# Kernel optimization log

Measured on AMD Instinct MI355X. Metric: run time of the kernel, lower is better.

The kernel has to match this reference:

```python
import jax, jax.numpy as jnp
import numpy as np

D_MODEL, HEAD_DIM = 1024, 128

def setup_inputs() -> dict:
    key = jax.random.key(0)
    kx, kq, kk, kv = jax.random.split(key, 4)
    x = jax.random.normal(kx, (4, 4096, D_MODEL), dtype=jnp.float32)
    s = 1.0 / np.sqrt(D_MODEL)
    Wq = jax.random.normal(kq, (D_MODEL, HEAD_DIM), dtype=jnp.float32) * s
    Wk = jax.random.normal(kk, (D_MODEL, HEAD_DIM), dtype=jnp.float32) * s
    Wv = jax.random.normal(kv, (D_MODEL, HEAD_DIM), dtype=jnp.float32) * s
    return {"x": x, "Wq": Wq, "Wk": Wk, "Wv": Wv}

def reference(x, Wq, Wk, Wv):
    # x: [b, s, d_model]; Wq/Wk/Wv: [d_model, head_dim]
    q = jnp.einsum('bsd,dh->bsh', x, Wq)
    k = jnp.einsum('bsd,dh->bsh', x, Wk)
    v = jnp.einsum('bsd,dh->bsh', x, Wv)
    seq = x.shape[1]
    scale = 1.0 / jnp.sqrt(jnp.asarray(q.shape[-1], q.dtype))
    scores = jnp.einsum('bqh,bkh->bqk', q, k) * scale  # [b, s, s]
    causal = jnp.tril(jnp.ones((seq, seq), dtype=bool))
    scores = jnp.where(causal, scores, jnp.asarray(-jnp.inf, scores.dtype))
    attn = jax.nn.softmax(scores, axis=-1)
    return jnp.einsum('bqk,bkh->bqh', attn, v)
```

## Files before the change

### kernel.cpp

```cpp
#include <hip/hip_runtime.h>
#include <hip/hip_bf16.h>
#include <math.h>

#define D_MODEL 1024
#define HD 128
#define SEQ 4096

typedef __bf16 bf16x8 __attribute__((ext_vector_type(8)));
typedef float f32x4 __attribute__((ext_vector_type(4)));
typedef unsigned int u32;
typedef u32 u32x4 __attribute__((ext_vector_type(4)));

__device__ __forceinline__ unsigned short f2bf(float f) {
    union { float f; u32 u; } c; c.f = f;
    u32 u = c.u;
    u = (u + 0x7fffu + ((u >> 16) & 1u)) >> 16;
    return (unsigned short)u;
}
__device__ __forceinline__ u32 pk2(float a, float b) {
    __hip_bfloat162 h = __float22bfloat162_rn(make_float2(a, b));
    union { __hip_bfloat162 h; u32 u; } c; c.h = h; return c.u;
}
__device__ __forceinline__ void dma16(void* lds, const void* g) {
    __builtin_amdgcn_global_load_lds(
        (const __attribute__((address_space(1))) u32*)g,
        (__attribute__((address_space(3))) u32*)lds, 16, 0, 0);
}
__device__ __forceinline__ void drain_dma()  { __builtin_amdgcn_s_waitcnt(0x0F70); }

__global__ __launch_bounds__(256)
void wt_kernel(const float* __restrict__ Wq, const float* __restrict__ Wk,
               const float* __restrict__ Wv, unsigned short* __restrict__ Wt) {
    __shared__ float wsf[64][129];
    const int t = threadIdx.x;
    const int k0 = blockIdx.x * 64;
    const int mat = blockIdx.y;
    const float* W = (mat == 0) ? Wq : (mat == 1) ? Wk : Wv;
    const float sc = (mat == 0) ? (0.08838834764831845f * 1.4426950408889634f) : 1.0f;
    {
        const int r = t >> 2, c = (t & 3) * 32;
        const float* src = W + (size_t)(k0 + r) * HD + c;
        #pragma unroll
        for (int j = 0; j < 32; j += 4)
            *reinterpret_cast<f32x4*>(&wsf[r][c + j]) = *reinterpret_cast<const f32x4*>(src + j);
    }
    __syncthreads();
    const int n = t >> 1, ks = (t & 1) * 32;
    u32 ow[16];
    #pragma unroll
    for (int j = 0; j < 16; ++j)
        ow[j] = pk2(wsf[ks + 2 * j][n] * sc, wsf[ks + 2 * j + 1][n] * sc);
    unsigned short* dst = Wt + (size_t)(mat * HD + n) * D_MODEL + k0 + ks;
    #pragma unroll
    for (int j = 0; j < 4; ++j)
        *reinterpret_cast<u32x4*>(dst + j * 8) = (u32x4){ow[4*j], ow[4*j+1], ow[4*j+2], ow[4*j+3]};
}

__global__ __launch_bounds__(512, 2)
void proj_kernel(const float* __restrict__ x, const unsigned short* __restrict__ Wt,
                 unsigned short* __restrict__ Qb, unsigned short* __restrict__ Kb,
                 unsigned short* __restrict__ Vt) {
    __shared__ __align__(1024) char ps[131072];
    const int t = threadIdx.x;
    const int w = t >> 6, l = t & 63, li = l & 15, g2 = l >> 4;
    const int mh = w >> 2, nq = w & 3;
    const int rowbase = blockIdx.x * 64;

    const int lr = l >> 3, lg = l & 7;
    const int cg = lg ^ lr;
    const int wn_add = (cg >> 2) * 192;
    const int wkq = (cg & 3) * 8;

    auto stage = [&](int it) {
        const int k0 = it * 32;
        const int buf = it & 3;
        dma16(ps + buf * 8192 + w * 1024,
              x + (size_t)(rowbase + w * 8 + lr) * D_MODEL + k0 + cg * 4);
        #pragma unroll
        for (int j = 0; j < 3; ++j) {
            int r0 = w * 24 + j * 8;
            dma16(ps + 32768 + buf * 24576 + r0 * 128,
                  Wt + (size_t)(r0 + lr + wn_add) * D_MODEL + k0 + wkq);
        }
    };

    f32x4 acc[2][6];
    #pragma unroll
    for (int mt = 0; mt < 2; ++mt)
        #pragma unroll
        for (int nt = 0; nt < 6; ++nt) acc[mt][nt] = (f32x4){0.f, 0.f, 0.f, 0.f};

    stage(0); stage(1); stage(2);
    for (int it = 0; it < 32; ++it) {
        if (it < 30)       __builtin_amdgcn_s_waitcnt(0x0F78);
        else if (it == 30) __builtin_amdgcn_s_waitcnt(0x0F74);
        else               drain_dma();
        __syncthreads();
        if (it + 3 < 32) stage(it + 3);

        const char* xb = ps + (it & 3) * 8192;
        const char* wb = ps + 32768 + (it & 3) * 24576;

        bf16x8 bf[6];
        #pragma unroll
        for (int nt = 0; nt < 6; ++nt) {
            int r = (nq & 1) * 96 + nt * 16 + li;
            bf[nt] = *reinterpret_cast<const bf16x8*>(
                wb + r * 128 + ((((nq >> 1) * 4 + g2) ^ (li & 7)) * 16));
        }
        #pragma unroll
        for (int mt = 0; mt < 2; ++mt) {
            int row = mh * 32 + mt * 16 + li;
            int p0 = ((2 * g2) ^ (li & 7)) * 16;
            f32x4 x0 = *reinterpret_cast<const f32x4*>(xb + row * 128 + p0);
            f32x4 x1 = *reinterpret_cast<const f32x4*>(xb + row * 128 + (p0 ^ 16));
            union { u32 d[4]; bf16x8 v; } cva;
            cva.d[0] = pk2(x0[0], x0[1]); cva.d[1] = pk2(x0[2], x0[3]);
            cva.d[2] = pk2(x1[0], x1[1]); cva.d[3] = pk2(x1[2], x1[3]);
            bf16x8 af = cva.v;
            #pragma unroll
            for (int nt = 0; nt < 6; ++nt)
                acc[mt][nt] = __builtin_amdgcn_mfma_f32_16x16x32_bf16(af, bf[nt], acc[mt][nt], 0, 0, 0);
        }
    }

    #pragma unroll
    for (int nt = 0; nt < 6; ++nt) {
        const int c0 = nq * 96 + nt * 16;
        #pragma unroll
        for (int mt = 0; mt < 2; ++mt) {
            const int m0 = mh * 32 + mt * 16 + g2 * 4;
            if (c0 < 256) {
                unsigned short* P = (c0 < 128) ? Qb : Kb;
                const int col = (c0 < 128 ? c0 : c0 - 128) + li;
                #pragma unroll
                for (int r = 0; r < 4; ++r)
                    P[(size_t)(rowbase + m0 + r) * HD + col] = f2bf(acc[mt][nt][r]);
            } else {
                const int d = c0 - 256 + li;
                const int b_ = rowbase >> 12, s_ = (rowbase + m0) & 4095;
                ushort4 s4;
                s4.x = f2bf(acc[mt][nt][0]); s4.y = f2bf(acc[mt][nt][1]);
                s4.z = f2bf(acc[mt][nt][2]); s4.w = f2bf(acc[mt][nt][3]);
                *reinterpret_cast<ushort4*>(&Vt[((size_t)b_ * HD + d) * SEQ + s_]) = s4;
            }
        }
    }
}

__global__ __launch_bounds__(256, 2)
void attn_kernel(const unsigned short* __restrict__ Qb, const unsigned short* __restrict__ Kb,
                 const unsigned short* __restrict__ Vt, float* __restrict__ outO,
                 unsigned short* __restrict__ Obf, float* __restrict__ Lbuf) {
    __shared__ __align__(1024) char smem[73728];
    const int t = threadIdx.x;
    const int w = t >> 6, l = t & 63, li = l & 15, g2 = l >> 4;
    const int qh = w >> 1, kh = w & 1;
    const int b = blockIdx.x & 3;
    const int u = blockIdx.x >> 2;
    const int g = 63 - (u >> 2);
    const int c = u & 3;
    const int R = g + 1;
    const int ts = (c * R) >> 2, te = ((c + 1) * R) >> 2;
    const int q0 = g * 64;
    const size_t rowb = (size_t)b * SEQ;
    const int koff = kh * 32;

    const unsigned short* KbB = Kb + rowb * HD;
    const unsigned short* VtB = Vt + (size_t)b * HD * SEQ;
    const int vgran = ((l & 7) ^ (l >> 3)) * 8;

    auto stage = [&](int it, char* base) {
        const int j0 = it * 64;
        #pragma unroll
        for (int j = 0; j < 4; ++j) {
            int rK = w * 16 + 4 * j + (l >> 4);
            dma16(base + (w * 16 + 4 * j) * 256,
                  KbB + (size_t)(j0 + rK) * 128 + (((l & 15) ^ (rK & 7)) * 8));
            int rV = w * 32 + 8 * j + (l >> 3);
            dma16(base + 16384 + (w * 32 + 8 * j) * 128,
                  VtB + (size_t)rV * SEQ + j0 + vgran);
        }
    };

    bf16x8 qf[2][4];
    #pragma unroll
    for (int qt = 0; qt < 2; ++qt)
        #pragma unroll
        for (int ks = 0; ks < 4; ++ks)
            qf[qt][ks] = *reinterpret_cast<const bf16x8*>(
                Qb + (rowb + q0 + qh * 32 + qt * 16 + li) * HD + ks * 32 + g2 * 8);

    f32x4 acco[2][8];
    #pragma unroll
    for (int qt = 0; qt < 2; ++qt)
        #pragma unroll
        for (int dt = 0; dt < 8; ++dt) acco[qt][dt] = (f32x4){0.f, 0.f, 0.f, 0.f};
    float ls[2] = {0.f, 0.f};

    const int gV = ((4 * kh + g2) ^ (li & 7)) * 16;

    if (ts < te) stage(ts, smem);
    for (int it = ts; it < te; ++it) {
        char* cbuf = smem + ((it - ts) & 1) * 32768;
        char* nbuf = smem + (((it - ts) & 1) ^ 1) * 32768;
        drain_dma();
        __syncthreads();
        if (it + 1 < te) stage(it + 1, nbuf);

        f32x4 accs[2][2];
        #pragma unroll
        for (int qt = 0; qt < 2; ++qt)
            #pragma unroll
            for (int kt = 0; kt < 2; ++kt) accs[qt][kt] = (f32x4){0.f, 0.f, 0.f, 0.f};
        #pragma unroll
        for (int kt = 0; kt < 2; ++kt) {
            const char* kb = cbuf + (koff + kt * 16 + li) * 256;
            #pragma unroll
            for (int ks = 0; ks < 4; ++ks) {
                bf16x8 kf = *reinterpret_cast<const bf16x8*>(kb + (((4 * ks + g2) ^ (li & 7)) * 16));
                accs[0][kt] = __builtin_amdgcn_mfma_f32_16x16x32_bf16(kf, qf[0][ks], accs[0][kt], 0, 0, 0);
                accs[1][kt] = __builtin_amdgcn_mfma_f32_16x16x32_bf16(kf, qf[1][ks], accs[1][kt], 0, 0, 0);
            }
        }

        const bool masked = (it == g);
        #pragma unroll
        for (int qt = 0; qt < 2; ++qt) {
            const int prow = qh * 32 + qt * 16 + li;
            #pragma unroll
            for (int kt = 0; kt < 2; ++kt) {
                float p[4];
                #pragma unroll
                for (int r = 0; r < 4; ++r) {
                    float s = accs[qt][kt][r];
                    if (masked && (koff + kt * 16 + g2 * 4 + r > prow)) s = -INFINITY;
                    p[r] = __builtin_amdgcn_exp2f(s - 16.0f);
                    ls[qt] += p[r];
                }
                union { u32 d[2]; uint2 v; } pw;
                pw.d[0] = pk2(p[0], p[1]); pw.d[1] = pk2(p[2], p[3]);
                int gr = (kh * 4 + kt * 2 + (g2 >> 1)) ^ (prow & 7);
                *reinterpret_cast<uint2*>(
                    smem + 65536 + prow * 128 + gr * 16 + (g2 & 1) * 8) = pw.v;
            }
        }

        bf16x8 pb[2];
        #pragma unroll
        for (int qt = 0; qt < 2; ++qt) {
            const int prow = qh * 32 + qt * 16 + li;
            pb[qt] = *reinterpret_cast<const bf16x8*>(
                smem + 65536 + prow * 128 + (((kh * 4 + g2) ^ (prow & 7)) * 16));
        }
        #pragma unroll
        for (int dt = 0; dt < 8; ++dt) {
            bf16x8 va = *reinterpret_cast<const bf16x8*>(cbuf + 16384 + (dt * 16 + li) * 128 + gV);
            acco[0][dt] = __builtin_amdgcn_mfma_f32_16x16x32_bf16(va, pb[0], acco[0][dt], 0, 0, 0);
            acco[1][dt] = __builtin_amdgcn_mfma_f32_16x16x32_bf16(va, pb[1], acco[1][dt], 0, 0, 0);
        }
    }

    #pragma unroll
    for (int qt = 0; qt < 2; ++qt) {
        ls[qt] += __shfl_xor(ls[qt], 16);
        ls[qt] += __shfl_xor(ls[qt], 32);
    }

    float (*Osum)[132] = (float(*)[132])smem;
    float* Lsh = (float*)(smem + 33792);
    __syncthreads();
    if (l < 16) {
        Lsh[kh * 64 + qh * 32 + l]      = ls[0];
        Lsh[kh * 64 + qh * 32 + 16 + l] = ls[1];
    }
    if (kh == 0) {
        #pragma unroll
        for (int qt = 0; qt < 2; ++qt)
            #pragma unroll
            for (int dt = 0; dt < 8; ++dt)
                *reinterpret_cast<f32x4*>(
                    &Osum[qh * 32 + qt * 16 + li][dt * 16 + g2 * 4]) = acco[qt][dt];
    }
    __syncthreads();
    if (kh == 1) {
        #pragma unroll
        for (int qt = 0; qt < 2; ++qt)
            #pragma unroll
            for (int dt = 0; dt < 8; ++dt) {
                f32x4* p = reinterpret_cast<f32x4*>(
                    &Osum[qh * 32 + qt * 16 + li][dt * 16 + g2 * 4]);
                f32x4 v = *p;
                #pragma unroll
                for (int j = 0; j < 4; ++j) v[j] += acco[qt][dt][j];
                *p = v;
            }
    }
    __syncthreads();

    if (t < 64)
        Lbuf[(size_t)c * 16384 + rowb + q0 + t] = Lsh[t] + Lsh[64 + t];
    #pragma unroll
    for (int k = 0; k < 8; ++k) {
        int idx = t + k * 256;
        int row = idx >> 5, col = (idx & 31) * 4;
        f32x4 o = *reinterpret_cast<const f32x4*>(&Osum[row][col]);
        size_t grow = rowb + q0 + row;
        if (c == 3) {
            *reinterpret_cast<f32x4*>(&outO[grow * HD + col]) = o;
        } else {
            union { u32 d[2]; uint2 v; } pkd;
            pkd.d[0] = pk2(o[0], o[1]); pkd.d[1] = pk2(o[2], o[3]);
            *reinterpret_cast<uint2*>(&Obf[(size_t)c * 2097152 + grow * HD + col]) = pkd.v;
        }
    }
}

__global__ __launch_bounds__(256)
void merge_kernel(float* __restrict__ outO, const unsigned short* __restrict__ Obf,
                  const float* __restrict__ Lbuf) {
    int tid = blockIdx.x * 256 + threadIdx.x;
    #pragma unroll
    for (int k = 0; k < 4; ++k) {
        int idx = tid + k * 131072;
        int row = idx >> 5, col = (idx & 31) * 4;
        float lsum = Lbuf[row] + Lbuf[16384 + row] + Lbuf[32768 + row] + Lbuf[49152 + row];
        float inv = 1.f / lsum;
        f32x4 o = *reinterpret_cast<const f32x4*>(&outO[(size_t)row * HD + col]);
        #pragma unroll
        for (int cc = 0; cc < 3; ++cc) {
            ushort4 uu = *reinterpret_cast<const ushort4*>(
                &Obf[(size_t)cc * 2097152 + (size_t)row * HD + col]);
            union { u32 u; float f; } a, b2, c2, d2;
            a.u = (u32)uu.x << 16; b2.u = (u32)uu.y << 16;
            c2.u = (u32)uu.z << 16; d2.u = (u32)uu.w << 16;
            o[0] += a.f; o[1] += b2.f; o[2] += c2.f; o[3] += d2.f;
        }
        #pragma unroll
        for (int j = 0; j < 4; ++j) o[j] *= inv;
        *reinterpret_cast<f32x4*>(&outO[(size_t)row * HD + col]) = o;
    }
}

extern "C" void kernel_launch(void* const* d_in, const int* in_sizes, int n_in,
                              void* d_out, int out_size, void* d_ws, size_t ws_size,
                              hipStream_t stream) {
    const float* x  = (const float*)d_in[0];
    const float* Wq = (const float*)d_in[1];
    const float* Wk = (const float*)d_in[2];
    const float* Wv = (const float*)d_in[3];
    float* out = (float*)d_out;

    char* ws = (char*)d_ws;
    unsigned short* Qb  = (unsigned short*)(ws);
    unsigned short* Kb  = (unsigned short*)(ws + ((size_t)4  << 20));
    unsigned short* Vt  = (unsigned short*)(ws + ((size_t)8  << 20));
    unsigned short* Wt  = (unsigned short*)(ws + ((size_t)12 << 20));
    unsigned short* Obf = (unsigned short*)(ws + ((size_t)13 << 20));
    float*          Lb  = (float*)(ws + ((size_t)25 << 20));

    wt_kernel   <<<dim3(16, 3), dim3(256), 0, stream>>>(Wq, Wk, Wv, Wt);
    proj_kernel <<<dim3(256),   dim3(512), 0, stream>>>(x, Wt, Qb, Kb, Vt);
    attn_kernel <<<dim3(1024),  dim3(256), 0, stream>>>(Qb, Kb, Vt, out, Obf, Lb);
    merge_kernel<<<dim3(512),   dim3(256), 0, stream>>>(out, Obf, Lb);
}
```

Measured before the change: 168.1 us.

## Retile projection to 128x192 blocks with register-staged bf16 x tiles

Measured after the change: 173.2 us. 3.0% more time.

```diff
diff --git a/kernel.cpp b/kernel.cpp
--- a/kernel.cpp
+++ b/kernel.cpp
@@ -60,85 +60,101 @@
 void proj_kernel(const float* __restrict__ x, const unsigned short* __restrict__ Wt,
                  unsigned short* __restrict__ Qb, unsigned short* __restrict__ Kb,
                  unsigned short* __restrict__ Vt) {
-    __shared__ __align__(1024) char ps[131072];
+    __shared__ __align__(1024) char ps[57344];
     const int t = threadIdx.x;
     const int w = t >> 6, l = t & 63, li = l & 15, g2 = l >> 4;
-    const int mh = w >> 2, nq = w & 3;
-    const int rowbase = blockIdx.x * 64;
+    const int mh = w >> 1, nq = w & 1;
+    const int rowbase = (blockIdx.x >> 1) * 128;
+    const int colbase = (blockIdx.x & 1) * 192;
 
     const int lr = l >> 3, lg = l & 7;
     const int cg = lg ^ lr;
-    const int wn_add = (cg >> 2) * 192;
+    const int wn_add = (cg >> 2) * 96;
     const int wkq = (cg & 3) * 8;
 
-    auto stage = [&](int it) {
+    auto stage_w = [&](int it) {
         const int k0 = it * 32;
-        const int buf = it & 3;
-        dma16(ps + buf * 8192 + w * 1024,
-              x + (size_t)(rowbase + w * 8 + lr) * D_MODEL + k0 + cg * 4);
+        char* wbs = ps + 20480 + (it % 3) * 12288;
         #pragma unroll
         for (int j = 0; j < 3; ++j) {
             int r0 = w * 24 + j * 8;
-            dma16(ps + 32768 + buf * 24576 + r0 * 128,
-                  Wt + (size_t)(r0 + lr + wn_add) * D_MODEL + k0 + wkq);
+            dma16(wbs + r0 * 128,
+                  Wt + (size_t)(colbase + r0 + lr + wn_add) * D_MODEL + k0 + wkq);
         }
     };
 
+    const float* xsrc = x + (size_t)(rowbase + w * 16 + (l >> 3)) * D_MODEL + (l & 7) * 4;
+    const int xwoff = (w * 16 + (l >> 3)) * 80 + (l & 7) * 8;
+
     f32x4 acc[2][6];
     #pragma unroll
     for (int mt = 0; mt < 2; ++mt)
         #pragma unroll
         for (int nt = 0; nt < 6; ++nt) acc[mt][nt] = (f32x4){0.f, 0.f, 0.f, 0.f};
 
-    stage(0); stage(1); stage(2);
+    {
+        f32x4 xv0 = *reinterpret_cast<const f32x4*>(xsrc);
+        f32x4 xv1 = *reinterpret_cast<const f32x4*>(xsrc + 8 * D_MODEL);
+        if (w < 4) { stage_w(0); stage_w(1); }
+        uint2 wv0 = {pk2(xv0[0], xv0[1]), pk2(xv0[2], xv0[3])};
+        uint2 wv1 = {pk2(xv1[0], xv1[1]), pk2(xv1[2], xv1[3])};
+        *reinterpret_cast<uint2*>(ps + xwoff) = wv0;
+        *reinterpret_cast<uint2*>(ps + 640 + xwoff) = wv1;
+    }
+
     for (int it = 0; it < 32; ++it) {
-        if (it < 30)       __builtin_amdgcn_s_waitcnt(0x0F78);
-        else if (it == 30) __builtin_amdgcn_s_waitcnt(0x0F74);
-        else               drain_dma();
+        if (w < 4) __builtin_amdgcn_s_waitcnt(0x0F73);
         __syncthreads();
-        if (it + 3 < 32) stage(it + 3);
-
-        const char* xb = ps + (it & 3) * 8192;
-        const char* wb = ps + 32768 + (it & 3) * 24576;
+
+        f32x4 xv0, xv1;
+        if (it + 1 < 32) {
+            const float* xs = xsrc + (it + 1) * 32;
+            xv0 = *reinterpret_cast<const f32x4*>(xs);
+            xv1 = *reinterpret_cast<const f32x4*>(xs + 8 * D_MODEL);
+        }
+        if (w < 4 && it + 2 < 32) stage_w(it + 2);
+
+        const char* xb = ps + (it & 1) * 10240;
+        const char* wb = ps + 20480 + (it % 3) * 12288;
 
         bf16x8 bf[6];
         #pragma unroll
-        for (int nt = 0; nt < 6; ++nt) {
-            int r = (nq & 1) * 96 + nt * 16 + li;
+        for (int nt = 0; nt < 6; ++nt)
             bf[nt] = *reinterpret_cast<const bf16x8*>(
-                wb + r * 128 + ((((nq >> 1) * 4 + g2) ^ (li & 7)) * 16));
-        }
+                wb + (nt * 16 + li) * 128 + (((nq * 4 + g2) ^ (li & 7)) * 16));
         #pragma unroll
         for (int mt = 0; mt < 2; ++mt) {
-            int row = mh * 32 + mt * 16 + li;
-            int p0 = ((2 * g2) ^ (li & 7)) * 16;
-            f32x4 x0 = *reinterpret_cast<const f32x4*>(xb + row * 128 + p0);
-            f32x4 x1 = *reinterpret_cast<const f32x4*>(xb + row * 128 + (p0 ^ 16));
-            union { u32 d[4]; bf16x8 v; } cva;
-            cva.d[0] = pk2(x0[0], x0[1]); cva.d[1] = pk2(x0[2], x0[3]);
-            cva.d[2] = pk2(x1[0], x1[1]); cva.d[3] = pk2(x1[2], x1[3]);
-            bf16x8 af = cva.v;
+            bf16x8 af = *reinterpret_cast<const bf16x8*>(
+                xb + (mh * 32 + mt * 16 + li) * 80 + g2 * 16);
             #pragma unroll
             for (int nt = 0; nt < 6; ++nt)
                 acc[mt][nt] = __builtin_amdgcn_mfma_f32_16x16x32_bf16(af, bf[nt], acc[mt][nt], 0, 0, 0);
         }
+
+        if (it + 1 < 32) {
+            char* xbn = ps + ((it + 1) & 1) * 10240;
+            uint2 wv0 = {pk2(xv0[0], xv0[1]), pk2(xv0[2], xv0[3])};
+            uint2 wv1 = {pk2(xv1[0], xv1[1]), pk2(xv1[2], xv1[3])};
+            *reinterpret_cast<uint2*>(xbn + xwoff) = wv0;
+            *reinterpret_cast<uint2*>(xbn + 640 + xwoff) = wv1;
+        }
     }
 
     #pragma unroll
     for (int nt = 0; nt < 6; ++nt) {
-        const int c0 = nq * 96 + nt * 16;
+        const int c0 = colbase + nq * 96 + nt * 16;
         #pragma unroll
         for (int mt = 0; mt < 2; ++mt) {
-            const int m0 = mh * 32 + mt * 16 + g2 * 4;
+            const int m0 = rowbase + mh * 32 + mt * 16 + g2 * 4;
             if (c0 < 256) {
                 unsigned short* P = (c0 < 128) ? Qb : Kb;
                 const int col = (c0 < 128 ? c0 : c0 - 128) + li;
                 #pragma unroll
                 for (int r = 0; r < 4; ++r)
-                    P[(size_t)(rowbase + m0 + r) * HD + col] = f2bf(acc[mt][nt][r]);
+                    P[(size_t)(m0 + r) * HD + col] = f2bf(acc[mt][nt][r]);
             } else {
                 const int d = c0 - 256 + li;
-                const int b_ = rowbase >> 12, s_ = (rowbase + m0) & 4095;
+                const int b_ = m0 >> 12, s_ = m0 & 4095;
                 ushort4 s4;
                 s4.x = f2bf(acc[mt][nt][0]); s4.y = f2bf(acc[mt][nt][1]);
                 s4.z = f2bf(acc[mt][nt][2]); s4.w = f2bf(acc[mt][nt][3]);
```
